# Performance work log

Hardware: AMD Instinct MI355X
Metric: run time of the kernel (lower is better)

Reference implementation:

```python
import jax, jax.numpy as jnp
import numpy as np


def setup_inputs() -> dict:
    key = jax.random.key(0)
    k1, k2, k3, k4 = jax.random.split(key, 4)
    B, C, H, W = 4, 256, 64, 64
    Va = jax.random.normal(k1, (B, C, H, W), jnp.float32)
    Vb = jax.random.normal(k2, (B, C, H, W), jnp.float32)
    # nn.Linear(C, C, bias=False) weight, used as x @ W^T
    W_linear = jax.random.normal(k3, (C, C), jnp.float32) * 0.05
    # nn.Conv2d(C, 1, 1, bias=False) weight, init normal_(0, 0.01)
    W_gate = jax.random.normal(k4, (C,), jnp.float32) * 0.01
    return {"Va_output": Va, "Vb_output": Vb, "W_linear": W_linear,
            "W_gate": W_gate, "input_size": 512}


def reference(Va_output, Vb_output, W_linear, W_gate, input_size):
    B, C, H, W = Vb_output.shape
    A = H * W  # all_dim
    Va_flat = Va_output.reshape(B, C, A)  # [B, C, A]
    Vb_flat = Vb_output.reshape(B, C, A)
    # linear on transposed A-major tokens: Va_t @ W_linear^T -> [B, A, C]
    Va_corr = jnp.einsum('bca,dc->bad', Va_flat, W_linear)
    # correlation matrix S = Va_corr @ Vb_flat -> [B, A, A]
    S = jnp.einsum('bac,can->ban'[:3] + 'c,c' if False else 'bac,cn', Va_corr, Vb_flat) if False else jnp.einsum('bac,bcn->ban', Va_corr, Vb_flat)
    # S_c = softmax(S, dim=1); S_r = softmax(S^T, dim=1) = softmax(S, axis=2)^T
    S_c = jax.nn.softmax(S, axis=1)
    S_r = jnp.swapaxes(jax.nn.softmax(S, axis=2), 1, 2)
    Vb_att = jnp.einsum('bca,ban->bcn', Va_flat, S_r).reshape(B, C, H, W)
    Va_att = jnp.einsum('bca,ban->bcn', Vb_flat, S_c).reshape(B, C, H, W)
    # 1x1 gate conv (C -> 1, no bias) + sigmoid
    Va_mask = jax.nn.sigmoid(jnp.einsum('bchw,c->bhw', Va_att, W_gate))[:, None]
    Vb_mask = jax.nn.sigmoid(jnp.einsum('bchw,c->bhw', Vb_att, W_gate))[:, None]
    Va_out = jnp.concatenate([Va_att * Va_mask, Va_output], axis=1)  # [B, 2C, H, W]
    Vb_out = jnp.concatenate([Vb_att * Vb_mask, Vb_output], axis=1)
    return (Va_out, Vb_out, input_size)
```

## Files before the change

### kernel.cpp

```cpp
#include <hip/hip_runtime.h>

typedef _Float16 f16;
typedef f16 f16x8 __attribute__((ext_vector_type(8)));
typedef float f32x4 __attribute__((ext_vector_type(4)));
typedef short b16x8 __attribute__((ext_vector_type(8)));
typedef unsigned short u16;
typedef u16 u16x4 __attribute__((ext_vector_type(4)));

#define MFMA_F16(a,b,c)  __builtin_amdgcn_mfma_f32_16x16x32_f16((a),(b),(c),0,0,0)
#define MFMA_BF16(a,b,c) __builtin_amdgcn_mfma_f32_16x16x32_bf16((a),(b),(c),0,0,0)

static __device__ __forceinline__ u16 bf16rn(float f) {
    unsigned u = __builtin_bit_cast(unsigned, f);
    u += 0x7FFFu + ((u >> 16) & 1u);
    return (u16)(u >> 16);
}

typedef const __attribute__((address_space(1))) unsigned int* gas_p;
typedef __attribute__((address_space(3))) unsigned int* las_p;
static __device__ __forceinline__ void gll16(const void* g, void* l) {
    __builtin_amdgcn_global_load_lds((gas_p)g, (las_p)l, 16, 0, 0);
}

static constexpr int B_ = 4, C_ = 256, A_ = 4096;
static constexpr int CA   = C_ * A_;
static constexpr int BCA  = B_ * CA;
static constexpr int OUT_T = B_ * 2 * CA;
static constexpr size_t WS_Va16 = 0;
static constexpr size_t WS_Vb16 = WS_Va16 + (size_t)BCA;
static constexpr size_t WS_VaT  = WS_Vb16 + (size_t)BCA;
static constexpr size_t WS_VbT  = WS_VaT  + (size_t)BCA;
static constexpr size_t WS_Q1   = WS_VbT  + (size_t)BCA;
static constexpr size_t WS_W16  = WS_Q1   + (size_t)BCA;
static constexpr size_t WS_HALFS = WS_W16 + (size_t)(C_ * C_);

static constexpr float M0 = 48.0f;

__global__ void coatt_convw(const float* __restrict__ W, f16* __restrict__ W16,
                            const int* __restrict__ psz, float* __restrict__ dout) {
    int i = blockIdx.x * 256 + threadIdx.x;
    W16[i] = (f16)W[i];
    if (i == 0) dout[16777216] = (float)(*psz);
}

__global__ void coatt_transpose(const float* __restrict__ Va,
                                const float* __restrict__ Vb,
                                u16* __restrict__ ws) {
    __shared__ f16 tile[64][73];
    int z = blockIdx.z; int b = z >> 1; int which = z & 1;
    const float* src = which ? Vb : Va;
    char* vt = (char*)(ws + (which ? WS_Vb16 : WS_Va16)) + (size_t)b * CA * 2;
    char* kt = (char*)(ws + (which ? WS_VbT : WS_VaT)) + (size_t)b * CA * 2;
    int a0 = blockIdx.x * 64, c0 = blockIdx.y * 64;
    int t = threadIdx.x;
    int r = t >> 2, q = t & 3;

    const float* sp = src + (size_t)(b * C_ + c0 + r) * A_ + a0 + q * 16;
    f16 h[16] __attribute__((aligned(16)));
    u16 hb[16] __attribute__((aligned(16)));
#pragma unroll
    for (int i = 0; i < 4; ++i) {
        float4 v = *(const float4*)(sp + i * 4);
        h[i*4+0] = (f16)v.x; h[i*4+1] = (f16)v.y;
        h[i*4+2] = (f16)v.z; h[i*4+3] = (f16)v.w;
        hb[i*4+0] = bf16rn(v.x); hb[i*4+1] = bf16rn(v.y);
        hb[i*4+2] = bf16rn(v.z); hb[i*4+3] = bf16rn(v.w);
    }
    char* vb8 = vt + (size_t)(a0 >> 6) * 32768 + (c0 + r) * 16;
    *(u16x4*)(vb8 + (q * 2 + 0) * 4096 + 0) = *(const u16x4*)&hb[0];
    *(u16x4*)(vb8 + (q * 2 + 0) * 4096 + 8) = *(const u16x4*)&hb[4];
    *(u16x4*)(vb8 + (q * 2 + 1) * 4096 + 0) = *(const u16x4*)&hb[8];
    *(u16x4*)(vb8 + (q * 2 + 1) * 4096 + 8) = *(const u16x4*)&hb[12];
#pragma unroll
    for (int i = 0; i < 16; ++i) tile[r][q * 16 + i] = h[i];
    __syncthreads();
    f16 ht[16] __attribute__((aligned(16)));
#pragma unroll
    for (int i = 0; i < 16; ++i) ht[i] = tile[q * 16 + i][r];
    char* kb8 = kt + (size_t)(a0 >> 6) * 32768 + r * 16;
    *(f16x8*)(kb8 + (size_t)(c0 / 8 + q * 2 + 0) * 1024) = *(const f16x8*)&ht[0];
    *(f16x8*)(kb8 + (size_t)(c0 / 8 + q * 2 + 1) * 1024) = *(const f16x8*)&ht[8];
}

__global__ __launch_bounds__(256) void coatt_q1(const u16* __restrict__ ws_) {
    const char* vat = (const char*)(ws_ + WS_VaT);
    const f16* w16 = (const f16*)(ws_ + WS_W16);
    char* q1 = (char*)(ws_ + WS_Q1);
    int b = blockIdx.y; int a0 = blockIdx.x * 64;
    int tid = threadIdx.x, wave = tid >> 6, lane = tid & 63;
    int m = lane & 15, quad = lane >> 4;

    const char* Ab = vat + (size_t)b * CA * 2 + (size_t)(a0 >> 6) * 32768;
    f16x8 af[8];
#pragma unroll
    for (int kc = 0; kc < 8; ++kc)
        af[kc] = *(const f16x8*)(Ab + (kc * 4 + quad) * 1024 + (wave * 16 + m) * 16);

    f32x4 acc[16];
#pragma unroll
    for (int t = 0; t < 16; ++t) acc[t] = (f32x4){0.f, 0.f, 0.f, 0.f};

#pragma unroll
    for (int kc = 0; kc < 8; ++kc) {
#pragma unroll
        for (int t = 0; t < 16; ++t) {
            f16x8 bf = *(const f16x8*)(w16 + (size_t)(t * 16 + m) * C_ + kc * 32 + quad * 8);
            acc[t] = MFMA_F16(af[kc], bf, acc[t]);
        }
    }
    char* Qb = q1 + (size_t)b * CA * 2 + (size_t)(a0 >> 6) * 32768;
#pragma unroll
    for (int t = 0; t < 16; ++t) {
#pragma unroll
        for (int r = 0; r < 4; ++r) {
            int al = wave * 16 + quad * 4 + r;
            int d = t * 16 + m;
            f16 v = (f16)acc[t][r];
            *(u16*)(Qb + (size_t)(d >> 3) * 1024 + al * 16 + (d & 7) * 2) =
                __builtin_bit_cast(u16, v);
        }
    }
}

__global__ __launch_bounds__(512, 2) void coatt_flash(const u16* __restrict__ ws,
                                                      const float* __restrict__ Wgate,
                                                      const float* __restrict__ Va,
                                                      const float* __restrict__ Vb,
                                                      float* __restrict__ dout) {
    __shared__ __align__(16) char smem[163840];
    char* Plds = smem + 131072;
    float* Lsum = (float*)(smem + 131072);
    float* Gsum = (float*)(smem + 131072 + 2048);
    float* Olds = (float*)smem;

    int p = blockIdx.x;
    int vc = p & 7;
    int b = vc & 3, att = vc >> 2;
    int n0 = (p >> 3) * 128;

    const char *Qp, *Kp, *Vp; float* outp;
    const char* base = (const char*)ws;
    size_t boff = (size_t)b * CA * 2;
    if (att == 0) {
        Qp = base + WS_Q1 * 2 + boff;
        Kp = base + WS_VbT * 2 + boff;
        Vp = base + WS_Va16 * 2 + boff;
        outp = dout + (size_t)OUT_T + (size_t)b * 2 * CA;
    } else {
        Qp = base + WS_VbT * 2 + boff;
        Kp = base + WS_Q1 * 2 + boff;
        Vp = base + WS_Vb16 * 2 + boff;
        outp = dout + (size_t)b * 2 * CA;
    }

    int tid = threadIdx.x, wave = tid >> 6, lane = tid & 63;
    int iq = wave >> 2, jq = wave & 3;
    int m = lane & 15, quad = lane >> 4;

    f16x8 qf[4][8];
    {
        const char* qb = Qp + (size_t)((n0 >> 6) + iq) * 32768;
#pragma unroll
        for (int qt = 0; qt < 4; ++qt)
#pragma unroll
            for (int kc = 0; kc < 8; ++kc)
                qf[qt][kc] = *(const f16x8*)(qb + (kc * 4 + quad) * 1024 +
                                             (qt * 16 + m) * 16);
    }

    f32x4 Oacc[4][4];
#pragma unroll
    for (int qt = 0; qt < 4; ++qt)
#pragma unroll
        for (int ct = 0; ct < 4; ++ct) Oacc[qt][ct] = (f32x4){0.f, 0.f, 0.f, 0.f};
    float lpart[4] = {0.f, 0.f, 0.f, 0.f};

    const char* ksrc = Kp + wave * 1024 + lane * 16;
    const char* vsrc = Vp + wave * 1024 + lane * 16;

    int pswz = m & 7;
    int pw_off = ((jq * 2 + (quad >> 1)) ^ pswz) * 16 + (quad & 1) * 8;
    int pr_off0 = ((0 * 4 + quad) ^ pswz) * 16;
    int pr_off1 = ((1 * 4 + quad) ^ pswz) * 16;

#pragma unroll
    for (int ii = 0; ii < 4; ++ii)
        gll16(ksrc + ii * 8192, smem + wave * 1024 + ii * 8192);
    __syncthreads();

    for (int kb = 0; kb < 64; ++kb) {
        int cur = kb & 1, nxt = cur ^ 1;
        char* Kc = smem + cur * 32768;
        char* Pw = Plds + cur * 16384;

        if (kb < 63) {
            const char* kg = ksrc + (size_t)(kb + 1) * 32768;
            char* kl = smem + nxt * 32768 + wave * 1024;
#pragma unroll
            for (int ii = 0; ii < 4; ++ii) gll16(kg + ii * 8192, kl + ii * 8192);
        }
        {
            const char* vg = vsrc + (size_t)kb * 32768;
            char* vl = smem + 65536 + cur * 32768 + wave * 1024;
#pragma unroll
            for (int ii = 0; ii < 4; ++ii) gll16(vg + ii * 8192, vl + ii * 8192);
        }

        f32x4 Sc[4];
#pragma unroll
        for (int qt = 0; qt < 4; ++qt) Sc[qt] = (f32x4){0.f, 0.f, 0.f, 0.f};
#pragma unroll
        for (int kc = 0; kc < 8; ++kc) {
            f16x8 kf = *(const f16x8*)(Kc + (kc * 4 + quad) * 1024 +
                                       (jq * 16 + m) * 16);
#pragma unroll
            for (int qt = 0; qt < 4; ++qt)
                Sc[qt] = MFMA_F16(kf, qf[qt][kc], Sc[qt]);
        }

#pragma unroll
        for (int qt = 0; qt < 4; ++qt) {
            int q = iq * 64 + qt * 16 + m;
            u16x4 pk;
            float s4 = 0.f;
#pragma unroll
            for (int r = 0; r < 4; ++r) {
                float pv = __expf(Sc[qt][r] - M0);
                s4 += pv;
                pk[r] = bf16rn(pv);
            }
            lpart[qt] += s4;
            *(u16x4*)(Pw + q * 128 + pw_off) = pk;
        }

        if (kb > 0) {
            char* Pr = Plds + nxt * 16384;
            char* Vr = smem + 65536 + nxt * 32768;
#pragma unroll
            for (int s = 0; s < 2; ++s) {
                int pro = s ? pr_off1 : pr_off0;
                b16x8 pf[4];
#pragma unroll
                for (int qt = 0; qt < 4; ++qt) {
                    int q = iq * 64 + qt * 16 + m;
                    pf[qt] = *(const b16x8*)(Pr + q * 128 + pro);
                }
#pragma unroll
                for (int ct = 0; ct < 4; ++ct) {
                    int c = jq * 64 + ct * 16 + m;
                    b16x8 vf = *(const b16x8*)(Vr + (s * 4 + quad) * 4096 + c * 16);
#pragma unroll
                    for (int qt = 0; qt < 4; ++qt)
                        Oacc[qt][ct] = MFMA_BF16(pf[qt], vf, Oacc[qt][ct]);
                }
            }
        }

        __syncthreads();
    }

    {
        char* Pr = Plds + 16384;
        char* Vr = smem + 65536 + 32768;
#pragma unroll
        for (int s = 0; s < 2; ++s) {
            int pro = s ? pr_off1 : pr_off0;
            b16x8 pf[4];
#pragma unroll
            for (int qt = 0; qt < 4; ++qt) {
                int q = iq * 64 + qt * 16 + m;
                pf[qt] = *(const b16x8*)(Pr + q * 128 + pro);
            }
#pragma unroll
            for (int ct = 0; ct < 4; ++ct) {
                int c = jq * 64 + ct * 16 + m;
                b16x8 vf = *(const b16x8*)(Vr + (s * 4 + quad) * 4096 + c * 16);
#pragma unroll
                for (int qt = 0; qt < 4; ++qt)
                    Oacc[qt][ct] = MFMA_BF16(pf[qt], vf, Oacc[qt][ct]);
            }
        }
    }

#pragma unroll
    for (int qt = 0; qt < 4; ++qt) {
        float v = lpart[qt];
        v += __shfl_xor(v, 16);
        v += __shfl_xor(v, 32);
        lpart[qt] = v;
    }
    __syncthreads();
    if (lane < 16) {
#pragma unroll
        for (int qt = 0; qt < 4; ++qt)
            Lsum[wave * 64 + qt * 16 + lane] = lpart[qt];
    }
    __syncthreads();
    float inv[4][4];
#pragma unroll
    for (int qt = 0; qt < 4; ++qt)
#pragma unroll
        for (int r = 0; r < 4; ++r) {
            int ql = qt * 16 + quad * 4 + r;
            float s = Lsum[(iq * 4 + 0) * 64 + ql] + Lsum[(iq * 4 + 1) * 64 + ql] +
                      Lsum[(iq * 4 + 2) * 64 + ql] + Lsum[(iq * 4 + 3) * 64 + ql];
            inv[qt][r] = 1.0f / s;
        }
    float gp[4][4] = {{0,0,0,0},{0,0,0,0},{0,0,0,0},{0,0,0,0}};
#pragma unroll
    for (int ct = 0; ct < 4; ++ct) {
        float w = Wgate[jq * 64 + ct * 16 + m];
#pragma unroll
        for (int qt = 0; qt < 4; ++qt)
#pragma unroll
            for (int r = 0; r < 4; ++r) {
                float o = Oacc[qt][ct][r] * inv[qt][r];
                Oacc[qt][ct][r] = o;
                gp[qt][r] += o * w;
            }
    }
#pragma unroll
    for (int qt = 0; qt < 4; ++qt)
#pragma unroll
        for (int r = 0; r < 4; ++r) {
            float v = gp[qt][r];
            v += __shfl_xor(v, 1); v += __shfl_xor(v, 2);
            v += __shfl_xor(v, 4); v += __shfl_xor(v, 8);
            gp[qt][r] = v;
        }
    if (m == 0) {
#pragma unroll
        for (int qt = 0; qt < 4; ++qt)
#pragma unroll
            for (int r = 0; r < 4; ++r)
                Gsum[wave * 64 + qt * 16 + quad * 4 + r] = gp[qt][r];
    }
    __syncthreads();
#pragma unroll
    for (int qt = 0; qt < 4; ++qt)
#pragma unroll
        for (int r = 0; r < 4; ++r) {
            int ql = qt * 16 + quad * 4 + r;
            float g = Gsum[(iq * 4 + 0) * 64 + ql] + Gsum[(iq * 4 + 1) * 64 + ql] +
                      Gsum[(iq * 4 + 2) * 64 + ql] + Gsum[(iq * 4 + 3) * 64 + ql];
            float msk = 1.0f / (1.0f + __expf(-g));
#pragma unroll
            for (int ct = 0; ct < 4; ++ct) Oacc[qt][ct][r] *= msk;
        }

    for (int hf = 0; hf < 2; ++hf) {
        __syncthreads();
        if ((jq >> 1) == hf) {
#pragma unroll
            for (int ct = 0; ct < 4; ++ct)
#pragma unroll
                for (int qt = 0; qt < 4; ++qt) {
                    int cl = (jq & 1) * 64 + ct * 16 + m;
                    float4 v;
                    v.x = Oacc[qt][ct][0]; v.y = Oacc[qt][ct][1];
                    v.z = Oacc[qt][ct][2]; v.w = Oacc[qt][ct][3];
                    *(float4*)(Olds + cl * 132 + iq * 64 + qt * 16 + quad * 4) = v;
                }
        }
        __syncthreads();
#pragma unroll
        for (int ii = 0; ii < 8; ++ii) {
            int ci = tid + ii * 512;
            int c = ci >> 5, ch = (ci & 31) * 4;
            float4 v = *(const float4*)(Olds + c * 132 + ch);
            *(float4*)(outp + (size_t)(hf * 128 + c) * A_ + n0 + ch) = v;
        }
    }

    {
        const float* rs = (att ? Va : Vb) + (size_t)b * CA;
        float* rdst = outp + (size_t)CA;
#pragma unroll
        for (int ii = 0; ii < 16; ++ii) {
            int i = tid + ii * 512;
            int c = i >> 5, off = (i & 31) * 4;
            float4 v = *(const float4*)(rs + (size_t)c * A_ + n0 + off);
            *(float4*)(rdst + (size_t)c * A_ + n0 + off) = v;
        }
    }
}

extern "C" void kernel_launch(void* const* d_in, const int* in_sizes, int n_in,
                              void* d_out, int out_size, void* d_ws, size_t ws_size,
                              hipStream_t stream) {
    const float* Va = (const float*)d_in[0];
    const float* Vb = (const float*)d_in[1];
    const float* Wl = (const float*)d_in[2];
    const float* Wg = (const float*)d_in[3];
    const int* psz  = (const int*)d_in[4];
    float* out = (float*)d_out;
    u16* ws = (u16*)d_ws;

    if (ws_size < WS_HALFS * sizeof(u16)) return;

    coatt_convw<<<256, 256, 0, stream>>>(Wl, (f16*)(ws + WS_W16), psz, out);
    coatt_transpose<<<dim3(64, 4, 8), 256, 0, stream>>>(Va, Vb, ws);
    coatt_q1<<<dim3(64, 4), 256, 0, stream>>>(ws);
    coatt_flash<<<256, 512, 0, stream>>>(ws, Wg, Va, Vb, out);
}
```

Measured before the change: 258.7 us.

## Fuse transpose/convert with Q1 projection GEMM into a single prep kernel

Merges the fp32-to-f16/bf16 transpose kernel and the Q1 linear projection kernel into one kernel. For Va blocks, the transposed tile stays in LDS and feeds MFMAs directly, so the VaT workspace round trip through global memory and one launch are removed. Each block now loops over all four channel tiles instead of using a separate grid dimension, which cuts the grid from 2048 to 512 blocks and may reduce parallelism during the prep phase.

```diff
diff --git a/kernel.cpp b/kernel.cpp
--- a/kernel.cpp
+++ b/kernel.cpp
@@ -43,81 +43,85 @@
     if (i == 0) dout[16777216] = (float)(*psz);
 }
 
-__global__ void coatt_transpose(const float* __restrict__ Va,
-                                const float* __restrict__ Vb,
-                                u16* __restrict__ ws) {
+__global__ __launch_bounds__(256) void coatt_prep(const float* __restrict__ Va,
+                                                  const float* __restrict__ Vb,
+                                                  const f16* __restrict__ w16,
+                                                  u16* __restrict__ ws) {
     __shared__ f16 tile[64][73];
-    int z = blockIdx.z; int b = z >> 1; int which = z & 1;
+    __shared__ f16 tile2[64][72];
+    int z = blockIdx.y; int b = z >> 1; int which = z & 1;
     const float* src = which ? Vb : Va;
     char* vt = (char*)(ws + (which ? WS_Vb16 : WS_Va16)) + (size_t)b * CA * 2;
-    char* kt = (char*)(ws + (which ? WS_VbT : WS_VaT)) + (size_t)b * CA * 2;
-    int a0 = blockIdx.x * 64, c0 = blockIdx.y * 64;
+    char* kt = (char*)(ws + WS_VbT) + (size_t)b * CA * 2;
+    int a0 = blockIdx.x * 64;
     int t = threadIdx.x;
     int r = t >> 2, q = t & 3;
-
-    const float* sp = src + (size_t)(b * C_ + c0 + r) * A_ + a0 + q * 16;
-    f16 h[16] __attribute__((aligned(16)));
-    u16 hb[16] __attribute__((aligned(16)));
-#pragma unroll
-    for (int i = 0; i < 4; ++i) {
-        float4 v = *(const float4*)(sp + i * 4);
-        h[i*4+0] = (f16)v.x; h[i*4+1] = (f16)v.y;
-        h[i*4+2] = (f16)v.z; h[i*4+3] = (f16)v.w;
-        hb[i*4+0] = bf16rn(v.x); hb[i*4+1] = bf16rn(v.y);
-        hb[i*4+2] = bf16rn(v.z); hb[i*4+3] = bf16rn(v.w);
-    }
-    char* vb8 = vt + (size_t)(a0 >> 6) * 32768 + (c0 + r) * 16;
-    *(u16x4*)(vb8 + (q * 2 + 0) * 4096 + 0) = *(const u16x4*)&hb[0];
-    *(u16x4*)(vb8 + (q * 2 + 0) * 4096 + 8) = *(const u16x4*)&hb[4];
-    *(u16x4*)(vb8 + (q * 2 + 1) * 4096 + 0) = *(const u16x4*)&hb[8];
-    *(u16x4*)(vb8 + (q * 2 + 1) * 4096 + 8) = *(const u16x4*)&hb[12];
-#pragma unroll
-    for (int i = 0; i < 16; ++i) tile[r][q * 16 + i] = h[i];
-    __syncthreads();
-    f16 ht[16] __attribute__((aligned(16)));
-#pragma unroll
-    for (int i = 0; i < 16; ++i) ht[i] = tile[q * 16 + i][r];
-    char* kb8 = kt + (size_t)(a0 >> 6) * 32768 + r * 16;
-    *(f16x8*)(kb8 + (size_t)(c0 / 8 + q * 2 + 0) * 1024) = *(const f16x8*)&ht[0];
-    *(f16x8*)(kb8 + (size_t)(c0 / 8 + q * 2 + 1) * 1024) = *(const f16x8*)&ht[8];
-}
-
-__global__ __launch_bounds__(256) void coatt_q1(const u16* __restrict__ ws_) {
-    const char* vat = (const char*)(ws_ + WS_VaT);
-    const f16* w16 = (const f16*)(ws_ + WS_W16);
-    char* q1 = (char*)(ws_ + WS_Q1);
-    int b = blockIdx.y; int a0 = blockIdx.x * 64;
-    int tid = threadIdx.x, wave = tid >> 6, lane = tid & 63;
-    int m = lane & 15, quad = lane >> 4;
-
-    const char* Ab = vat + (size_t)b * CA * 2 + (size_t)(a0 >> 6) * 32768;
-    f16x8 af[8];
-#pragma unroll
-    for (int kc = 0; kc < 8; ++kc)
-        af[kc] = *(const f16x8*)(Ab + (kc * 4 + quad) * 1024 + (wave * 16 + m) * 16);
+    int wave = t >> 6, lane = t & 63, m = lane & 15, quad = lane >> 4;
 
     f32x4 acc[16];
 #pragma unroll
-    for (int t = 0; t < 16; ++t) acc[t] = (f32x4){0.f, 0.f, 0.f, 0.f};
-
-#pragma unroll
-    for (int kc = 0; kc < 8; ++kc) {
-#pragma unroll
-        for (int t = 0; t < 16; ++t) {
-            f16x8 bf = *(const f16x8*)(w16 + (size_t)(t * 16 + m) * C_ + kc * 32 + quad * 8);
-            acc[t] = MFMA_F16(af[kc], bf, acc[t]);
-        }
-    }
-    char* Qb = q1 + (size_t)b * CA * 2 + (size_t)(a0 >> 6) * 32768;
-#pragma unroll
-    for (int t = 0; t < 16; ++t) {
-#pragma unroll
-        for (int r = 0; r < 4; ++r) {
-            int al = wave * 16 + quad * 4 + r;
-            int d = t * 16 + m;
-            f16 v = (f16)acc[t][r];
-            *(u16*)(Qb + (size_t)(d >> 3) * 1024 + al * 16 + (d & 7) * 2) =
-                __builtin_bit_cast(u16, v);
+    for (int i = 0; i < 16; ++i) acc[i] = (f32x4){0.f, 0.f, 0.f, 0.f};
+
+    for (int ct = 0; ct < 4; ++ct) {
+        int c0 = ct * 64;
+        const float* sp = src + (size_t)(b * C_ + c0 + r) * A_ + a0 + q * 16;
+        f16 h[16] __attribute__((aligned(16)));
+        u16 hb[16] __attribute__((aligned(16)));
+#pragma unroll
+        for (int i = 0; i < 4; ++i) {
+            float4 v = *(const float4*)(sp + i * 4);
+            h[i*4+0] = (f16)v.x; h[i*4+1] = (f16)v.y;
+            h[i*4+2] = (f16)v.z; h[i*4+3] = (f16)v.w;
+            hb[i*4+0] = bf16rn(v.x); hb[i*4+1] = bf16rn(v.y);
+            hb[i*4+2] = bf16rn(v.z); hb[i*4+3] = bf16rn(v.w);
+        }
+        char* vb8 = vt + (size_t)(a0 >> 6) * 32768 + (c0 + r) * 16;
+        *(u16x4*)(vb8 + (q * 2 + 0) * 4096 + 0) = *(const u16x4*)&hb[0];
+        *(u16x4*)(vb8 + (q * 2 + 0) * 4096 + 8) = *(const u16x4*)&hb[4];
+        *(u16x4*)(vb8 + (q * 2 + 1) * 4096 + 0) = *(const u16x4*)&hb[8];
+        *(u16x4*)(vb8 + (q * 2 + 1) * 4096 + 8) = *(const u16x4*)&hb[12];
+#pragma unroll
+        for (int i = 0; i < 16; ++i) tile[r][q * 16 + i] = h[i];
+        __syncthreads();
+        f16 ht[16] __attribute__((aligned(16)));
+#pragma unroll
+        for (int i = 0; i < 16; ++i) ht[i] = tile[q * 16 + i][r];
+        if (which) {
+            char* kb8 = kt + (size_t)(a0 >> 6) * 32768 + r * 16;
+            *(f16x8*)(kb8 + (size_t)(c0 / 8 + q * 2 + 0) * 1024) = *(const f16x8*)&ht[0];
+            *(f16x8*)(kb8 + (size_t)(c0 / 8 + q * 2 + 1) * 1024) = *(const f16x8*)&ht[8];
+        } else {
+            *(f16x8*)&tile2[r][q * 16]     = *(const f16x8*)&ht[0];
+            *(f16x8*)&tile2[r][q * 16 + 8] = *(const f16x8*)&ht[8];
+        }
+        __syncthreads();
+        if (!which) {
+#pragma unroll
+            for (int kc = 0; kc < 2; ++kc) {
+                f16x8 af = *(const f16x8*)&tile2[wave * 16 + m][kc * 32 + quad * 8];
+#pragma unroll
+                for (int tt = 0; tt < 16; ++tt) {
+                    f16x8 bf = *(const f16x8*)(w16 + (size_t)(tt * 16 + m) * C_ +
+                                               c0 + kc * 32 + quad * 8);
+                    acc[tt] = MFMA_F16(af, bf, acc[tt]);
+                }
+            }
+        }
+    }
+
+    if (!which) {
+        char* Qb = (char*)(ws + WS_Q1) + (size_t)b * CA * 2 +
+                   (size_t)(a0 >> 6) * 32768;
+#pragma unroll
+        for (int tt = 0; tt < 16; ++tt) {
+#pragma unroll
+            for (int rr = 0; rr < 4; ++rr) {
+                int al = wave * 16 + quad * 4 + rr;
+                int d = tt * 16 + m;
+                f16 v = (f16)acc[tt][rr];
+                *(u16*)(Qb + (size_t)(d >> 3) * 1024 + al * 16 + (d & 7) * 2) =
+                    __builtin_bit_cast(u16, v);
+            }
         }
     }
 }
@@ -399,7 +403,6 @@
     if (ws_size < WS_HALFS * sizeof(u16)) return;
 
     coatt_convw<<<256, 256, 0, stream>>>(Wl, (f16*)(ws + WS_W16), psz, out);
-    coatt_transpose<<<dim3(64, 4, 8), 256, 0, stream>>>(Va, Vb, ws);
-    coatt_q1<<<dim3(64, 4), 256, 0, stream>>>(ws);
+    coatt_prep<<<dim3(64, 8), 256, 0, stream>>>(Va, Vb, (const f16*)(ws + WS_W16), ws);
     coatt_flash<<<256, 512, 0, stream>>>(ws, Wg, Va, Vb, out);
 }
```

Result: slower. 270.1 us (+4.4%).
